# Kernel tuning notes

Hardware: AMD Instinct MI355X
Metric: run time of the kernel (lower is better)

Reference implementation:

```python
import jax, jax.numpy as jnp
import numpy as np

N = 100000  # nodes
E = 600000  # edges
NUM_REL = 2

def _lrelu(v):
    return jax.nn.leaky_relu(v, negative_slope=0.01)

def _rgcn_layer(x, src, dst, rel_masks, W_root, W_rel, b):
    # PyG RGCNConv (aggr='mean'): out = x @ W_root + sum_r mean_{edges of rel r into i}(x_src @ W_r) + b
    n = x.shape[0]
    out = x @ W_root + b
    for r in range(NUM_REL):
        m = rel_masks[r]  # [E] float 0/1
        xr = x @ W_rel[r]                      # [N,128]
        msg = xr[src] * m[:, None]             # [E,128]
        agg = jax.ops.segment_sum(msg, dst, num_segments=n)   # [N,128]
        cnt = jax.ops.segment_sum(m, dst, num_segments=n)     # [N]
        out = out + agg / jnp.maximum(cnt, 1.0)[:, None]
    return out

def setup_inputs() -> dict:
    key = jax.random.key(0)
    ks = jax.random.split(key, 24)
    def p(k, shape, scale=0.05):
        return jax.random.normal(k, shape, dtype=jnp.float32) * scale
    inp = {
        'des': p(ks[0], (N, 768), 1.0),
        'tweet': p(ks[1], (N, 768), 1.0),
        'num_prop': p(ks[2], (N, 7), 1.0),
        'cat_prop': p(ks[3], (N, 11), 1.0),
        'new_feature': p(ks[4], (N, 1), 1.0),
        'edge_index': jax.random.randint(ks[5], (2, E), 0, N),
        'edge_type': jax.random.randint(ks[6], (E,), 0, NUM_REL),
        'W_des': p(ks[7], (768, 28)), 'b_des': jnp.zeros((28,), jnp.float32),
        'W_tweet': p(ks[8], (768, 36)), 'b_tweet': jnp.zeros((36,), jnp.float32),
        'W_num': p(ks[9], (7, 12)), 'b_num': jnp.zeros((12,), jnp.float32),
        'W_cat': p(ks[10], (11, 40)), 'b_cat': jnp.zeros((40,), jnp.float32),
        'W_new': p(ks[11], (1, 12)), 'b_new': jnp.zeros((12,), jnp.float32),
        'W_in': p(ks[12], (128, 128)), 'b_in': jnp.zeros((128,), jnp.float32),
        'W_root': p(ks[13], (4, 128, 128)),
        'W_rel': p(ks[14], (4, NUM_REL, 128, 128)),
        'b_rgcn': jnp.zeros((4, 128), jnp.float32),
        'W_o1': p(ks[15], (128, 128)), 'b_o1': jnp.zeros((128,), jnp.float32),
        'W_o2': p(ks[16], (128, 2)), 'b_o2': jnp.zeros((2,), jnp.float32),
    }
    return inp

def reference(des, tweet, num_prop, cat_prop, new_feature, edge_index, edge_type,
              W_des, b_des, W_tweet, b_tweet, W_num, b_num, W_cat, b_cat,
              W_new, b_new, W_in, b_in, W_root, W_rel, b_rgcn, W_o1, b_o1, W_o2, b_o2):
    d = _lrelu(des @ W_des + b_des)
    t = _lrelu(tweet @ W_tweet + b_tweet)
    n = _lrelu(num_prop @ W_num + b_num)
    c = _lrelu(cat_prop @ W_cat + b_cat)
    nf = _lrelu(new_feature @ W_new + b_new)
    x = jnp.concatenate([d, t, n, c, nf], axis=1)   # [N,128]
    x = _lrelu(x @ W_in + b_in)
    src, dst = edge_index[0], edge_index[1]
    rel_masks = [(edge_type == r).astype(x.dtype) for r in range(NUM_REL)]
    for i in range(4):  # dropout is identity in eval mode
        x = _rgcn_layer(x, src, dst, rel_masks, W_root[i], W_rel[i], b_rgcn[i])
    x = _lrelu(x @ W_o1 + b_o1)
    return x @ W_o2 + b_o2  # [N,2]
```

## Files before the change

### kernel.cpp

```cpp
#include <hip/hip_runtime.h>

typedef __attribute__((ext_vector_type(8))) short short8;
typedef __attribute__((ext_vector_type(4))) float floatx4;

__device__ inline void split_bf16(float v, unsigned short &h, unsigned short &l) {
    unsigned u = __float_as_uint(v);
    unsigned hu = (u + 0x8000u) & 0xFFFF0000u;
    h = (unsigned short)(hu >> 16);
    float lf = v - __uint_as_float(hu);
    l = (unsigned short)(__float_as_uint(lf) >> 16);
}

#define BN 64
#define BK 32

__global__ __launch_bounds__(256) void enc_big_kernel(
    const float* __restrict__ des, const float* __restrict__ tweet,
    const float* __restrict__ Wd, const float* __restrict__ bd,
    const float* __restrict__ Wt, const float* __restrict__ bt,
    float* __restrict__ out, int n)
{
    __shared__ float Xd[BN][BK + 4];
    __shared__ float Xt[BN][BK + 4];
    __shared__ float Wl[BK][64];
    int n0 = blockIdx.x * BN;
    int cg = threadIdx.x & 15;
    int rg = threadIdx.x >> 4;

    float acc[4][4];
#pragma unroll
    for (int a = 0; a < 4; a++)
#pragma unroll
        for (int b = 0; b < 4; b++) acc[a][b] = 0.f;

    for (int k0 = 0; k0 < 768; k0 += BK) {
        __syncthreads();
#pragma unroll
        for (int p = 0; p < 2; p++) {
            int idx = threadIdx.x + p * 256;
            int row = idx >> 3, kq = idx & 7;
            int gr = n0 + row; if (gr > n - 1) gr = n - 1;
            float4 vd = *(const float4*)(des   + (size_t)gr * 768 + k0 + kq * 4);
            float4 vt = *(const float4*)(tweet + (size_t)gr * 768 + k0 + kq * 4);
            *(float4*)&Xd[row][kq * 4] = vd;
            *(float4*)&Xt[row][kq * 4] = vt;
        }
#pragma unroll
        for (int p = 0; p < 2; p++) {
            int idx = threadIdx.x + p * 256;
            int k = idx >> 4, cq = idx & 15;
            float4 w;
            if (cq < 7) w = *(const float4*)(Wd + (size_t)(k0 + k) * 28 + cq * 4);
            else        w = *(const float4*)(Wt + (size_t)(k0 + k) * 36 + (cq - 7) * 4);
            *(float4*)&Wl[k][cq * 4] = w;
        }
        __syncthreads();

        const float* xb = (cg < 7) ? &Xd[0][0] : &Xt[0][0];
#pragma unroll 4
        for (int k = 0; k < BK; k++) {
            float4 w = *(const float4*)&Wl[k][cg * 4];
#pragma unroll
            for (int rr = 0; rr < 4; rr++) {
                float xv = xb[(rg * 4 + rr) * (BK + 4) + k];
                acc[rr][0] += xv * w.x;
                acc[rr][1] += xv * w.y;
                acc[rr][2] += xv * w.z;
                acc[rr][3] += xv * w.w;
            }
        }
    }

    float bb[4];
#pragma unroll
    for (int c = 0; c < 4; c++) {
        int j = cg * 4 + c;
        bb[c] = (j < 28) ? bd[j] : bt[j - 28];
    }
#pragma unroll
    for (int rr = 0; rr < 4; rr++) {
        int r = n0 + rg * 4 + rr;
        if (r < n) {
            float4 o;
            o.x = acc[rr][0] + bb[0];
            o.y = acc[rr][1] + bb[1];
            o.z = acc[rr][2] + bb[2];
            o.w = acc[rr][3] + bb[3];
            o.x = o.x > 0.f ? o.x : 0.01f * o.x;
            o.y = o.y > 0.f ? o.y : 0.01f * o.y;
            o.z = o.z > 0.f ? o.z : 0.01f * o.z;
            o.w = o.w > 0.f ? o.w : 0.01f * o.w;
            *(float4*)(out + (size_t)r * 128 + cg * 4) = o;
        }
    }
}

__global__ __launch_bounds__(256) void enc_small_kernel(
    const float* __restrict__ nump, const float* __restrict__ catp,
    const float* __restrict__ nf,
    const float* __restrict__ Wn, const float* __restrict__ bn,
    const float* __restrict__ Wc, const float* __restrict__ bc,
    const float* __restrict__ Ww, const float* __restrict__ bw,
    float* __restrict__ out, int n)
{
    int node = blockIdx.x * 4 + (threadIdx.x >> 6);
    if (node >= n) return;
    int j = threadIdx.x & 63;
    float acc;
    if (j < 12) {
        acc = bn[j];
        for (int k = 0; k < 7; k++) acc += nump[(size_t)node * 7 + k] * Wn[k * 12 + j];
    } else if (j < 52) {
        int c = j - 12;
        acc = bc[c];
        for (int k = 0; k < 11; k++) acc += catp[(size_t)node * 11 + k] * Wc[k * 40 + c];
    } else {
        int c = j - 52;
        acc = bw[c] + nf[node] * Ww[c];
    }
    acc = acc > 0.f ? acc : 0.01f * acc;
    out[(size_t)node * 128 + 64 + j] = acc;
}

__global__ void prep_w_kernel(const float* __restrict__ src,
                              unsigned short* __restrict__ dh,
                              unsigned short* __restrict__ dl, int total)
{
    int idx = blockIdx.x * 256 + threadIdx.x;
    if (idx >= total) return;
    int m = idx >> 14, r = idx & 16383;
    int k = r >> 7, col = r & 127;
    unsigned short h, l;
    split_bf16(src[idx], h, l);
    int didx = (m << 14) | (col << 7) | k;
    dh[didx] = h; dl[didx] = l;
}

__global__ __launch_bounds__(256) void dense_mfma_kernel(
    const float* __restrict__ in0, const float* __restrict__ in1, const float* __restrict__ in2,
    int s0, int o0, int s1, int o1, int s2, int o2,
    const unsigned short* __restrict__ Wh, const unsigned short* __restrict__ Wl,
    int slot0, int slot1, int slot2,
    const float* __restrict__ bias, float* __restrict__ out,
    int nphases, int relu, int N)
{
    __shared__ unsigned short Xh[64][136];
    __shared__ unsigned short Xl[64][136];
    int base = blockIdx.x * 64;
    int lane = threadIdx.x & 63;
    int wv   = threadIdx.x >> 6;
    int srow = threadIdx.x >> 2;
    int sseg = threadIdx.x & 3;
    int mrow = lane & 15;
    int quad = lane >> 4;

    floatx4 acc[4][2];
#pragma unroll
    for (int t = 0; t < 4; t++)
#pragma unroll
        for (int ct = 0; ct < 2; ct++) acc[t][ct] = (floatx4){0.f, 0.f, 0.f, 0.f};

    for (int p = 0; p < nphases; p++) {
        const float* inp = (p == 0) ? in0 : (p == 1) ? in1 : in2;
        int st   = (p == 0) ? s0 : (p == 1) ? s1 : s2;
        int off  = (p == 0) ? o0 : (p == 1) ? o1 : o2;
        int slot = (p == 0) ? slot0 : (p == 1) ? slot1 : slot2;

        __syncthreads();
        {
            int gr = base + srow; if (gr >= N) gr = N - 1;
            const float* src = inp + (size_t)gr * st + off + sseg * 32;
            unsigned short th[32], tl[32];
#pragma unroll
            for (int q = 0; q < 8; q++) {
                float4 v = *(const float4*)(src + q * 4);
                split_bf16(v.x, th[q * 4 + 0], tl[q * 4 + 0]);
                split_bf16(v.y, th[q * 4 + 1], tl[q * 4 + 1]);
                split_bf16(v.z, th[q * 4 + 2], tl[q * 4 + 2]);
                split_bf16(v.w, th[q * 4 + 3], tl[q * 4 + 3]);
            }
#pragma unroll
            for (int q = 0; q < 4; q++) {
                *(short8*)&Xh[srow][sseg * 32 + q * 8] = *(short8*)&th[q * 8];
                *(short8*)&Xl[srow][sseg * 32 + q * 8] = *(short8*)&tl[q * 8];
            }
        }
        __syncthreads();

        const unsigned short* wh = Wh + (size_t)slot * 16384;
        const unsigned short* wl = Wl + (size_t)slot * 16384;
#pragma unroll
        for (int ks = 0; ks < 4; ks++) {
            int kk = ks * 32 + quad * 8;
            short8 ah[4], al[4];
#pragma unroll
            for (int t = 0; t < 4; t++) {
                ah[t] = *(const short8*)&Xh[t * 16 + mrow][kk];
                al[t] = *(const short8*)&Xl[t * 16 + mrow][kk];
            }
#pragma unroll
            for (int ct = 0; ct < 2; ct++) {
                int col = wv * 32 + ct * 16 + mrow;
                short8 bh = *(const short8*)(wh + col * 128 + kk);
                short8 bl = *(const short8*)(wl + col * 128 + kk);
#pragma unroll
                for (int t = 0; t < 4; t++) {
                    acc[t][ct] = __builtin_amdgcn_mfma_f32_16x16x32_bf16(ah[t], bh, acc[t][ct], 0, 0, 0);
                    acc[t][ct] = __builtin_amdgcn_mfma_f32_16x16x32_bf16(ah[t], bl, acc[t][ct], 0, 0, 0);
                    acc[t][ct] = __builtin_amdgcn_mfma_f32_16x16x32_bf16(al[t], bh, acc[t][ct], 0, 0, 0);
                }
            }
        }
    }

#pragma unroll
    for (int ct = 0; ct < 2; ct++) {
        int col = wv * 32 + ct * 16 + mrow;
        float bv = bias[col];
#pragma unroll
        for (int t = 0; t < 4; t++) {
#pragma unroll
            for (int rg = 0; rg < 4; rg++) {
                int r = base + t * 16 + quad * 4 + rg;
                if (r < N) {
                    float v = acc[t][ct][rg] + bv;
                    if (relu) v = v > 0.f ? v : 0.01f * v;
                    out[(size_t)r * 128 + col] = v;
                }
            }
        }
    }
}

__global__ void count_kernel(const int* __restrict__ ei, const int* __restrict__ et,
                             int* __restrict__ deg, int E, int N)
{
    int e = blockIdx.x * 256 + threadIdx.x;
    if (e < E) atomicAdd(&deg[(size_t)et[e] * N + ei[E + e]], 1);
}

__global__ void scan1_kernel(const int* __restrict__ deg, int* __restrict__ bsum, int m)
{
    int i = blockIdx.x * 256 + threadIdx.x;
    int v = (i < m) ? deg[i] : 0;
#pragma unroll
    for (int off = 32; off > 0; off >>= 1) v += __shfl_down(v, off);
    __shared__ int ws4[4];
    if ((threadIdx.x & 63) == 0) ws4[threadIdx.x >> 6] = v;
    __syncthreads();
    if (threadIdx.x == 0) bsum[blockIdx.x] = ws4[0] + ws4[1] + ws4[2] + ws4[3];
}

__global__ __launch_bounds__(1024) void scan2_kernel(int* __restrict__ bsum, int nb)
{
    __shared__ int s[1024];
    int t = threadIdx.x;
    int v = (t < nb) ? bsum[t] : 0;
    s[t] = v;
    __syncthreads();
    for (int off = 1; off < 1024; off <<= 1) {
        int u = 0;
        if (t >= off) u = s[t - off];
        __syncthreads();
        s[t] += u;
        __syncthreads();
    }
    if (t < nb) bsum[t] = s[t] - v;
}

__global__ void scan3_kernel(const int* __restrict__ deg, const int* __restrict__ bsum,
                             int* __restrict__ offs, int m)
{
    __shared__ int s[256];
    int i = blockIdx.x * 256 + threadIdx.x;
    int t = threadIdx.x;
    int v = (i < m) ? deg[i] : 0;
    s[t] = v;
    __syncthreads();
    for (int off = 1; off < 256; off <<= 1) {
        int u = 0;
        if (t >= off) u = s[t - off];
        __syncthreads();
        s[t] += u;
        __syncthreads();
    }
    if (i < m) offs[i] = bsum[blockIdx.x] + s[t] - v;
}

__global__ void fill_kernel(const int* __restrict__ ei, const int* __restrict__ et,
                            int* __restrict__ offs, int* __restrict__ ord, int E, int N)
{
    int e = blockIdx.x * 256 + threadIdx.x;
    if (e >= E) return;
    int b = et[e] * N + ei[E + e];
    int pos = atomicAdd(&offs[b], 1);
    ord[pos] = ei[e];
}

__global__ __launch_bounds__(256) void gather2_kernel(
    const float* __restrict__ x, const int* __restrict__ offs,
    const int* __restrict__ ord, float* __restrict__ G, int N)
{
    int d = blockIdx.x * 8 + (threadIdx.x >> 5);
    if (d >= N) return;
    int lane = threadIdx.x & 31;
#pragma unroll
    for (int r = 0; r < 2; r++) {
        int b = r * N + d;
        int end = offs[b];
        int beg = (b == 0) ? 0 : offs[b - 1];
        float4 acc = {0.f, 0.f, 0.f, 0.f};
        for (int p = beg; p < end; p++) {
            int s = ord[p];
            float4 v = *(const float4*)(x + (size_t)s * 128 + lane * 4);
            acc.x += v.x; acc.y += v.y; acc.z += v.z; acc.w += v.w;
        }
        int dg = end - beg;
        float invd = 1.0f / (float)(dg > 1 ? dg : 1);
        float4 o;
        o.x = acc.x * invd; o.y = acc.y * invd; o.z = acc.z * invd; o.w = acc.w * invd;
        *(float4*)(G + (size_t)d * 256 + r * 128 + lane * 4) = o;
    }
}

__global__ __launch_bounds__(256) void head_kernel(
    const float* __restrict__ y, const float* __restrict__ W2,
    const float* __restrict__ b2, float* __restrict__ out, int n)
{
    int node = blockIdx.x * 4 + (threadIdx.x >> 6);
    if (node >= n) return;
    int lane = threadIdx.x & 63;
    float x0 = y[(size_t)node * 128 + lane];
    float x1 = y[(size_t)node * 128 + 64 + lane];
    float s0 = x0 * W2[lane * 2]     + x1 * W2[(lane + 64) * 2];
    float s1 = x0 * W2[lane * 2 + 1] + x1 * W2[(lane + 64) * 2 + 1];
#pragma unroll
    for (int off = 32; off > 0; off >>= 1) {
        s0 += __shfl_down(s0, off);
        s1 += __shfl_down(s1, off);
    }
    if (lane == 0) {
        out[(size_t)node * 2]     = s0 + b2[0];
        out[(size_t)node * 2 + 1] = s1 + b2[1];
    }
}

extern "C" void kernel_launch(void* const* d_in, const int* in_sizes, int n_in,
                              void* d_out, int out_size, void* d_ws, size_t ws_size,
                              hipStream_t stream)
{
    const float* des   = (const float*)d_in[0];
    const float* tweet = (const float*)d_in[1];
    const float* nump  = (const float*)d_in[2];
    const float* catp  = (const float*)d_in[3];
    const float* nf    = (const float*)d_in[4];
    const int*   ei    = (const int*)d_in[5];
    const int*   et    = (const int*)d_in[6];
    const float* Wd  = (const float*)d_in[7],  *bd  = (const float*)d_in[8];
    const float* Wt  = (const float*)d_in[9],  *bt  = (const float*)d_in[10];
    const float* Wn  = (const float*)d_in[11], *bn  = (const float*)d_in[12];
    const float* Wc  = (const float*)d_in[13], *bc  = (const float*)d_in[14];
    const float* Ww  = (const float*)d_in[15], *bw  = (const float*)d_in[16];
    const float* Win = (const float*)d_in[17], *bin = (const float*)d_in[18];
    const float* Wroot = (const float*)d_in[19];
    const float* Wrel  = (const float*)d_in[20];
    const float* brg   = (const float*)d_in[21];
    const float* Wo1 = (const float*)d_in[22], *bo1 = (const float*)d_in[23];
    const float* Wo2 = (const float*)d_in[24], *bo2 = (const float*)d_in[25];

    int N = in_sizes[0] / 768;
    int E = in_sizes[6];

    float* x = (float*)d_ws;
    float* G = x + (size_t)N * 128;
    unsigned short* Wth = (unsigned short*)(G + (size_t)N * 256);
    unsigned short* Wtl = Wth + (size_t)14 * 16384;
    int* deg  = (int*)(Wtl + (size_t)14 * 16384);
    int* offs = deg + (size_t)2 * N;
    int* ord  = offs + (size_t)2 * N;
    int* bsum = ord + (size_t)E;

    int m = 2 * N;
    int nb = (m + 255) / 256;

    hipMemsetAsync(deg, 0, (size_t)m * sizeof(int), stream);

    prep_w_kernel<<<(16384 + 255) / 256, 256, 0, stream>>>(Win, Wth, Wtl, 16384);
    prep_w_kernel<<<(4 * 16384 + 255) / 256, 256, 0, stream>>>(Wroot, Wth + 1 * 16384, Wtl + 1 * 16384, 4 * 16384);
    prep_w_kernel<<<(8 * 16384 + 255) / 256, 256, 0, stream>>>(Wrel, Wth + 5 * 16384, Wtl + 5 * 16384, 8 * 16384);
    prep_w_kernel<<<(16384 + 255) / 256, 256, 0, stream>>>(Wo1, Wth + 13 * 16384, Wtl + 13 * 16384, 16384);

    enc_big_kernel<<<(N + BN - 1) / BN, 256, 0, stream>>>(
        des, tweet, Wd, bd, Wt, bt, x, N);
    enc_small_kernel<<<(N + 3) / 4, 256, 0, stream>>>(
        nump, catp, nf, Wn, bn, Wc, bc, Ww, bw, x, N);

    count_kernel<<<(E + 255) / 256, 256, 0, stream>>>(ei, et, deg, E, N);
    scan1_kernel<<<nb, 256, 0, stream>>>(deg, bsum, m);
    scan2_kernel<<<1, 1024, 0, stream>>>(bsum, nb);
    scan3_kernel<<<nb, 256, 0, stream>>>(deg, bsum, offs, m);
    fill_kernel<<<(E + 255) / 256, 256, 0, stream>>>(ei, et, offs, ord, E, N);

    int nblk = (N + 63) / 64;
    dense_mfma_kernel<<<nblk, 256, 0, stream>>>(
        x, x, x, 128, 0, 128, 0, 128, 0, Wth, Wtl, 0, 0, 0, bin, x, 1, 1, N);

    for (int i = 0; i < 4; i++) {
        gather2_kernel<<<(N + 7) / 8, 256, 0, stream>>>(x, offs, ord, G, N);
        dense_mfma_kernel<<<nblk, 256, 0, stream>>>(
            x, G, G, 128, 0, 256, 0, 256, 128,
            Wth, Wtl, 1 + i, 5 + 2 * i, 6 + 2 * i,
            brg + (size_t)i * 128, x, 3, 0, N);
    }

    dense_mfma_kernel<<<nblk, 256, 0, stream>>>(
        x, x, x, 128, 0, 128, 0, 128, 0, Wth, Wtl, 13, 13, 13, bo1, x, 1, 1, N);
    head_kernel<<<(N + 3) / 4, 256, 0, stream>>>(x, Wo2, bo2, (float*)d_out, N);
}
```

Before: 1.476 ms.

## Replace scalar FP32 encoder GEMM with split-bf16 MFMA kernel

Replaces the scalar FMA encoder for the des/tweet 768-wide projections with an MFMA kernel. Inputs are split into bf16 hi/lo in shared memory, and the weights are pre-split into a combined column-major 64x1536 layout by a new prep kernel that uses the G buffer as scratch. Three MFMAs per tile (hh, hl, lh) emulate fp32 accuracy. The aim is to cut compute time in this memory-heavy stage. In exchange it adds conversion work, idles waves on half the k-panels, and writes outputs with scalar stores.

After: 1.448 ms. Within noise of the previous version (-1.9%).

```diff
diff --git a/kernel.cpp b/kernel.cpp
--- a/kernel.cpp
+++ b/kernel.cpp
@@ -2,6 +2,7 @@
 
 typedef __attribute__((ext_vector_type(8))) short short8;
 typedef __attribute__((ext_vector_type(4))) float floatx4;
+typedef __attribute__((ext_vector_type(4))) unsigned short ushort4v;
 
 __device__ inline void split_bf16(float v, unsigned short &h, unsigned short &l) {
     unsigned u = __float_as_uint(v);
@@ -11,86 +12,101 @@
     l = (unsigned short)(__float_as_uint(lf) >> 16);
 }
 
-#define BN 64
-#define BK 32
-
-__global__ __launch_bounds__(256) void enc_big_kernel(
+__global__ void prep_wenc_kernel(const float* __restrict__ Wd, const float* __restrict__ Wt,
+                                 unsigned short* __restrict__ dh, unsigned short* __restrict__ dl)
+{
+    int col = blockIdx.x;
+    int k   = blockIdx.y * 256 + threadIdx.x;
+    float v;
+    if (col < 28) v = (k < 768)  ? Wd[(size_t)k * 28 + col] : 0.f;
+    else          v = (k >= 768) ? Wt[(size_t)(k - 768) * 36 + (col - 28)] : 0.f;
+    unsigned short h, l;
+    split_bf16(v, h, l);
+    dh[(size_t)col * 1536 + k] = h;
+    dl[(size_t)col * 1536 + k] = l;
+}
+
+__global__ __launch_bounds__(256, 4) void enc_mfma_kernel(
     const float* __restrict__ des, const float* __restrict__ tweet,
-    const float* __restrict__ Wd, const float* __restrict__ bd,
-    const float* __restrict__ Wt, const float* __restrict__ bt,
-    float* __restrict__ out, int n)
-{
-    __shared__ float Xd[BN][BK + 4];
-    __shared__ float Xt[BN][BK + 4];
-    __shared__ float Wl[BK][64];
-    int n0 = blockIdx.x * BN;
-    int cg = threadIdx.x & 15;
-    int rg = threadIdx.x >> 4;
-
-    float acc[4][4];
-#pragma unroll
-    for (int a = 0; a < 4; a++)
-#pragma unroll
-        for (int b = 0; b < 4; b++) acc[a][b] = 0.f;
-
-    for (int k0 = 0; k0 < 768; k0 += BK) {
-        __syncthreads();
-#pragma unroll
-        for (int p = 0; p < 2; p++) {
-            int idx = threadIdx.x + p * 256;
-            int row = idx >> 3, kq = idx & 7;
-            int gr = n0 + row; if (gr > n - 1) gr = n - 1;
-            float4 vd = *(const float4*)(des   + (size_t)gr * 768 + k0 + kq * 4);
-            float4 vt = *(const float4*)(tweet + (size_t)gr * 768 + k0 + kq * 4);
-            *(float4*)&Xd[row][kq * 4] = vd;
-            *(float4*)&Xt[row][kq * 4] = vt;
-        }
-#pragma unroll
-        for (int p = 0; p < 2; p++) {
-            int idx = threadIdx.x + p * 256;
-            int k = idx >> 4, cq = idx & 15;
-            float4 w;
-            if (cq < 7) w = *(const float4*)(Wd + (size_t)(k0 + k) * 28 + cq * 4);
-            else        w = *(const float4*)(Wt + (size_t)(k0 + k) * 36 + (cq - 7) * 4);
-            *(float4*)&Wl[k][cq * 4] = w;
-        }
-        __syncthreads();
-
-        const float* xb = (cg < 7) ? &Xd[0][0] : &Xt[0][0];
-#pragma unroll 4
-        for (int k = 0; k < BK; k++) {
-            float4 w = *(const float4*)&Wl[k][cg * 4];
-#pragma unroll
-            for (int rr = 0; rr < 4; rr++) {
-                float xv = xb[(rg * 4 + rr) * (BK + 4) + k];
-                acc[rr][0] += xv * w.x;
-                acc[rr][1] += xv * w.y;
-                acc[rr][2] += xv * w.z;
-                acc[rr][3] += xv * w.w;
-            }
-        }
-    }
-
-    float bb[4];
-#pragma unroll
-    for (int c = 0; c < 4; c++) {
-        int j = cg * 4 + c;
-        bb[c] = (j < 28) ? bd[j] : bt[j - 28];
-    }
-#pragma unroll
-    for (int rr = 0; rr < 4; rr++) {
-        int r = n0 + rg * 4 + rr;
-        if (r < n) {
-            float4 o;
-            o.x = acc[rr][0] + bb[0];
-            o.y = acc[rr][1] + bb[1];
-            o.z = acc[rr][2] + bb[2];
-            o.w = acc[rr][3] + bb[3];
-            o.x = o.x > 0.f ? o.x : 0.01f * o.x;
-            o.y = o.y > 0.f ? o.y : 0.01f * o.y;
-            o.z = o.z > 0.f ? o.z : 0.01f * o.z;
-            o.w = o.w > 0.f ? o.w : 0.01f * o.w;
-            *(float4*)(out + (size_t)r * 128 + cg * 4) = o;
+    const unsigned short* __restrict__ Wh, const unsigned short* __restrict__ Wl,
+    const float* __restrict__ bd, const float* __restrict__ bt,
+    float* __restrict__ out, int N)
+{
+    __shared__ unsigned short Xh[64][136];
+    __shared__ unsigned short Xl[64][136];
+    int base = blockIdx.x * 64;
+    int lane = threadIdx.x & 63;
+    int wv   = threadIdx.x >> 6;
+    int srow = threadIdx.x >> 2;
+    int sseg = threadIdx.x & 3;
+    int mrow = lane & 15;
+    int quad = lane >> 4;
+
+    floatx4 acc[4];
+#pragma unroll
+    for (int t = 0; t < 4; t++) acc[t] = (floatx4){0.f, 0.f, 0.f, 0.f};
+
+    for (int p = 0; p < 12; p++) {
+        const float* inp = (p < 6) ? des : tweet;
+        int k0 = (p < 6) ? p * 128 : (p - 6) * 128;
+
+        __syncthreads();
+        {
+            int gr = base + srow; if (gr >= N) gr = N - 1;
+            const float* src = inp + (size_t)gr * 768 + k0 + sseg * 32;
+#pragma unroll
+            for (int q = 0; q < 8; q++) {
+                float4 v = *(const float4*)(src + q * 4);
+                unsigned short h0, h1, h2, h3, l0, l1, l2, l3;
+                split_bf16(v.x, h0, l0);
+                split_bf16(v.y, h1, l1);
+                split_bf16(v.z, h2, l2);
+                split_bf16(v.w, h3, l3);
+                ushort4v hv = {h0, h1, h2, h3};
+                ushort4v lv = {l0, l1, l2, l3};
+                *(ushort4v*)&Xh[srow][sseg * 32 + q * 4] = hv;
+                *(ushort4v*)&Xl[srow][sseg * 32 + q * 4] = lv;
+            }
+        }
+        __syncthreads();
+
+        bool active = (wv == 1) || ((wv == 0) ? (p < 6) : (p >= 6));
+        if (active) {
+            const unsigned short* wh = Wh + (size_t)(wv * 16 + mrow) * 1536 + p * 128;
+            const unsigned short* wl = Wl + (size_t)(wv * 16 + mrow) * 1536 + p * 128;
+#pragma unroll
+            for (int ks = 0; ks < 4; ks++) {
+                int kk = ks * 32 + quad * 8;
+                short8 ah[4], al[4];
+#pragma unroll
+                for (int t = 0; t < 4; t++) {
+                    ah[t] = *(const short8*)&Xh[t * 16 + mrow][kk];
+                    al[t] = *(const short8*)&Xl[t * 16 + mrow][kk];
+                }
+                short8 bh = *(const short8*)(wh + kk);
+                short8 bl = *(const short8*)(wl + kk);
+#pragma unroll
+                for (int t = 0; t < 4; t++) {
+                    acc[t] = __builtin_amdgcn_mfma_f32_16x16x32_bf16(ah[t], bh, acc[t], 0, 0, 0);
+                    acc[t] = __builtin_amdgcn_mfma_f32_16x16x32_bf16(ah[t], bl, acc[t], 0, 0, 0);
+                    acc[t] = __builtin_amdgcn_mfma_f32_16x16x32_bf16(al[t], bh, acc[t], 0, 0, 0);
+                }
+            }
+        }
+    }
+
+    int col = wv * 16 + mrow;
+    float bv = (col < 28) ? bd[col] : bt[col - 28];
+#pragma unroll
+    for (int t = 0; t < 4; t++) {
+#pragma unroll
+        for (int rg = 0; rg < 4; rg++) {
+            int r = base + t * 16 + quad * 4 + rg;
+            if (r < N) {
+                float v = acc[t][rg] + bv;
+                v = v > 0.f ? v : 0.01f * v;
+                out[(size_t)r * 128 + col] = v;
+            }
         }
     }
 }
@@ -380,8 +396,12 @@
     int* ord  = offs + (size_t)2 * N;
     int* bsum = ord + (size_t)E;
 
+    unsigned short* WEh = (unsigned short*)G;
+    unsigned short* WEl = WEh + (size_t)64 * 1536;
+
     int m = 2 * N;
     int nb = (m + 255) / 256;
+    int nblk = (N + 63) / 64;
 
     hipMemsetAsync(deg, 0, (size_t)m * sizeof(int), stream);
 
@@ -389,9 +409,9 @@
     prep_w_kernel<<<(4 * 16384 + 255) / 256, 256, 0, stream>>>(Wroot, Wth + 1 * 16384, Wtl + 1 * 16384, 4 * 16384);
     prep_w_kernel<<<(8 * 16384 + 255) / 256, 256, 0, stream>>>(Wrel, Wth + 5 * 16384, Wtl + 5 * 16384, 8 * 16384);
     prep_w_kernel<<<(16384 + 255) / 256, 256, 0, stream>>>(Wo1, Wth + 13 * 16384, Wtl + 13 * 16384, 16384);
-
-    enc_big_kernel<<<(N + BN - 1) / BN, 256, 0, stream>>>(
-        des, tweet, Wd, bd, Wt, bt, x, N);
+    prep_wenc_kernel<<<dim3(64, 6), 256, 0, stream>>>(Wd, Wt, WEh, WEl);
+
+    enc_mfma_kernel<<<nblk, 256, 0, stream>>>(des, tweet, WEh, WEl, bd, bt, x, N);
     enc_small_kernel<<<(N + 3) / 4, 256, 0, stream>>>(
         nump, catp, nf, Wn, bn, Wc, bc, Ww, bw, x, N);
 
@@ -401,7 +421,6 @@
     scan3_kernel<<<nb, 256, 0, stream>>>(deg, bsum, offs, m);
     fill_kernel<<<(E + 255) / 256, 256, 0, stream>>>(ei, et, offs, ord, E, N);
 
-    int nblk = (N + 63) / 64;
     dense_mfma_kernel<<<nblk, 256, 0, stream>>>(
         x, x, x, 128, 0, 128, 0, 128, 0, Wth, Wtl, 0, 0, 0, bin, x, 1, 1, N);
 
```
